# Kernel optimization log

Hardware: AMD Instinct MI355X
Metric: run time of the kernel (lower is better)

The kernel has to match this reference:

```python
import jax, jax.numpy as jnp
import numpy as np

B, T, K, H = 2, 2048, 1024, 16


def setup_inputs() -> dict:
    key = jax.random.key(0)
    ks = jax.random.split(key, 9)
    sc = 0.02
    return {
        "x": jax.random.normal(ks[0], (B, T, K), dtype=jnp.float32),
        "Wq_w": jax.random.normal(ks[1], (K, K), dtype=jnp.float32) * sc,
        "Wq_b": jax.random.normal(ks[2], (K,), dtype=jnp.float32) * sc,
        "Wk_w": jax.random.normal(ks[3], (K, K), dtype=jnp.float32) * sc,
        "Wk_b": jax.random.normal(ks[4], (K,), dtype=jnp.float32) * sc,
        "Wv_w": jax.random.normal(ks[5], (K, K), dtype=jnp.float32) * sc,
        "Wv_b": jax.random.normal(ks[6], (K,), dtype=jnp.float32) * sc,
        "Wo_w": jax.random.normal(ks[7], (K, K), dtype=jnp.float32) * sc,
        "Wo_b": jax.random.normal(ks[8], (K,), dtype=jnp.float32) * sc,
    }


def reference(x, Wq_w, Wq_b, Wk_w, Wk_b, Wv_w, Wv_b, Wo_w, Wo_b):
    b, t, k = x.shape
    h = H
    s = k // h
    # nn.Linear: y = x @ W^T + b
    q = x @ Wq_w.T + Wq_b
    kk = x @ Wk_w.T + Wk_b
    v = x @ Wv_w.T + Wv_b
    # [b, t, h, s] -> [b, h, t, s]
    q = q.reshape(b, t, h, s).transpose(0, 2, 1, 3)
    kk = kk.reshape(b, t, h, s).transpose(0, 2, 1, 3)
    v = v.reshape(b, t, h, s).transpose(0, 2, 1, 3)
    # scores [b, h, t, t]
    dot = jnp.einsum("bhqd,bhkd->bhqk", q, kk)
    # causal mask: upper triangle (offset=1) set to -inf BEFORE scaling
    causal = jnp.tril(jnp.ones((t, t), dtype=bool))
    dot = jnp.where(causal, dot, -jnp.inf)
    # NOTE: original scales by sqrt(k) (full model dim), not sqrt(head_dim)
    dot = dot / jnp.sqrt(jnp.asarray(k, dot.dtype))
    attn = jax.nn.softmax(dot, axis=-1)
    out = jnp.einsum("bhqk,bhkd->bhqd", attn, v)  # [b, h, t, s]
    out = out.transpose(0, 2, 1, 3).reshape(b, t, k)
    return out @ Wo_w.T + Wo_b
```

## Files before the change

kernel.cpp:

```cpp
#include <hip/hip_runtime.h>

typedef unsigned short u16;
typedef unsigned int u32;
typedef __bf16 bf16x8 __attribute__((ext_vector_type(8)));
typedef float f32x4 __attribute__((ext_vector_type(4)));
typedef unsigned short u16x8 __attribute__((ext_vector_type(8)));
typedef unsigned int u32x4 __attribute__((ext_vector_type(4)));

#define B_ 2
#define T_ 2048
#define K_ 1024
#define H_ 16
#define S_ 64
#define MKC 4194304
#define QSCALE 0.04508422f

__device__ __forceinline__ u16 f2bf(float f) {
  unsigned int u = __builtin_bit_cast(unsigned int, f);
  u += 0x7fffu + ((u >> 16) & 1u);
  return (u16)(u >> 16);
}

__device__ __forceinline__ f32x4 MFMA(bf16x8 a, bf16x8 b, f32x4 c) {
  return __builtin_amdgcn_mfma_f32_16x16x32_bf16(a, b, c, 0, 0, 0);
}

__device__ __forceinline__ void gld16(const void* g, void* l) {
  __builtin_amdgcn_global_load_lds((const __attribute__((address_space(1))) void*)g,
                                   (__attribute__((address_space(3))) void*)l, 16, 0, 0);
}

template <int N>
__device__ __forceinline__ void waitv() {
  asm volatile("s_waitcnt vmcnt(%0)" ::"i"(N) : "memory");
}
__device__ __forceinline__ void memfence_barrier() {
  asm volatile("" ::: "memory");
  __builtin_amdgcn_s_barrier();
}

__global__ __launch_bounds__(256) void cvt_all(const float* __restrict__ x,
                                               const float* __restrict__ W0,
                                               const float* __restrict__ W1,
                                               const float* __restrict__ W2,
                                               const float* __restrict__ W3,
                                               u16* __restrict__ xb,
                                               u16* __restrict__ wb) {
  const int i = blockIdx.x * 256 + threadIdx.x;
  const float* src;
  u16* dst;
  if (i < 524288) {
    src = x + (size_t)i * 8;
    dst = xb + (size_t)i * 8;
  } else {
    const int j = i - 524288;
    const int sel = j >> 17;
    const float* W = sel == 0 ? W0 : sel == 1 ? W1 : sel == 2 ? W2 : W3;
    src = W + (size_t)(j & 131071) * 8;
    dst = wb + (size_t)j * 8;
  }
  const float4* s = (const float4*)src;
  float4 f0 = s[0], f1 = s[1];
  u16x8 p;
  p[0] = f2bf(f0.x); p[1] = f2bf(f0.y); p[2] = f2bf(f0.z); p[3] = f2bf(f0.w);
  p[4] = f2bf(f1.x); p[5] = f2bf(f1.y); p[6] = f2bf(f1.z); p[7] = f2bf(f1.w);
  *(u16x8*)dst = p;
}

template <int OMODE, int BN>
__global__ __launch_bounds__(256) void gemm16(const u16* __restrict__ A,
                                              const u16* __restrict__ Bm,
                                              const float* __restrict__ b0,
                                              const float* __restrict__ b1,
                                              const float* __restrict__ b2,
                                              void* __restrict__ C0,
                                              int M, int N, int K) {
  constexpr int NF = BN / 32;
  constexpr int SOPS = 2 + BN / 64;
  __shared__ u16 As[2][128 * 32];
  __shared__ u16 Bs[2][BN * 32];
  const int bm = blockIdx.x * 128;
  const int bn = blockIdx.y * BN;
  const int tid = threadIdx.x;
  const int w = tid >> 6, lane = tid & 63;
  const int wr = (w >> 1) * 64, wc = (w & 1) * (BN / 2);
  const int lr = lane & 15, g = lane >> 4;
  const int lk = (g ^ ((lr >> 1) & 3)) * 8;
  const int srow = lane >> 2;
  const int scol = ((lane & 3) ^ ((lane >> 3) & 3)) * 8;

  f32x4 acc[4][NF] = {};

  auto stg = [&](int buf, int k0) {
#pragma unroll
    for (int i = 0; i < 2; ++i) {
      const int rbase = (i * 4 + w) * 16;
      gld16(A + (size_t)(bm + rbase + srow) * K + k0 + scol, &As[buf][rbase * 32]);
    }
#pragma unroll
    for (int i = 0; i < BN / 64; ++i) {
      const int rbase = (i * 4 + w) * 16;
      gld16(Bm + (size_t)(bn + rbase + srow) * K + k0 + scol, &Bs[buf][rbase * 32]);
    }
  };

  stg(0, 0);
  const int NK = K >> 5;
  for (int kk = 0; kk < NK; ++kk) {
    const int buf = kk & 1;
    const bool pf = (kk + 1 < NK);
    if (pf) {
      stg(buf ^ 1, (kk + 1) * 32);
      waitv<SOPS>();
    } else {
      waitv<0>();
    }
    __builtin_amdgcn_s_barrier();
    bf16x8 af[4], bfr[NF];
#pragma unroll
    for (int m = 0; m < 4; ++m)
      af[m] = *(const bf16x8*)&As[buf][(wr + m * 16 + lr) * 32 + lk];
#pragma unroll
    for (int n = 0; n < NF; ++n)
      bfr[n] = *(const bf16x8*)&Bs[buf][(wc + n * 16 + lr) * 32 + lk];
#pragma unroll
    for (int m = 0; m < 4; ++m)
#pragma unroll
      for (int n = 0; n < NF; ++n)
        acc[m][n] = MFMA(af[m], bfr[n], acc[m][n]);
    memfence_barrier();
  }

  const int sel = (OMODE == 2) ? 0 : (bn >> 10);
  const float* bp = (OMODE == 2) ? b0 : (sel == 0 ? b0 : sel == 1 ? b1 : b2);
#pragma unroll
  for (int n = 0; n < NF; ++n) {
    const int col = bn + wc + n * 16 + lr;
    const float bv = bp[(OMODE == 2) ? col : (col & 1023)];
#pragma unroll
    for (int m = 0; m < 4; ++m) {
#pragma unroll
      for (int r = 0; r < 4; ++r) {
        const int row = bm + wr + m * 16 + g * 4 + r;
        float v = acc[m][n][r] + bv;
        if (OMODE == 2) {
          ((float*)C0)[(size_t)row * N + col] = v;
        } else {
          u16* dst = (u16*)C0;
          const int cc = col & 1023;
          if (sel == 2) {
            const int bb = row >> 11, t = row & 2047, hh = cc >> 6, ss = cc & 63;
            dst[(size_t)2 * MKC + (((size_t)(bb * H_ + hh) * S_ + ss) << 11) + t] = f2bf(v);
          } else {
            if (sel == 0) v *= QSCALE;
            dst[(size_t)sel * MKC + (size_t)row * 1024 + cc] = f2bf(v);
          }
        }
      }
    }
  }
}

__global__ __launch_bounds__(256) void attn_fwd(const u16* __restrict__ Q,
                                                const u16* __restrict__ Kb,
                                                const u16* __restrict__ Vt,
                                                u16* __restrict__ O) {
  __shared__ u16 Ks[2][64 * 64];
  __shared__ u16 Vs[2][64 * 64];
  const int tid = threadIdx.x;
  const int w = tid >> 6, lane = tid & 63;
  const int qh = lane & 15;
  const int g = lane >> 4;
  const int bh = blockIdx.x;
  const int b = bh >> 4, h = bh & 15;
  const int yy = blockIdx.y;

  const int srow = lane >> 3;
  const int sl8 = ((lane & 7) ^ srow) * 8;
  int kvp[2];
#pragma unroll
  for (int i = 0; i < 2; ++i) {
    const int rho = w * 16 + i * 8 + srow;
    const int a = rho >> 4;
    kvp[i] = ((a >> 1) << 5) | (((rho >> 2) & 3) << 3) | ((a & 1) << 2) | (rho & 3);
  }
  const int ksw = qh & 7;
  u16x8 ov;
#pragma unroll
  for (int i = 0; i < 8; ++i) ov[i] = 0x3F80;
  const bf16x8 ones = __builtin_bit_cast(bf16x8, ov);

  for (int seg = 0; seg < 2; ++seg) {
    const int qtile = seg ? (31 - yy) : yy;
    const int qb = qtile * 64;
    const int qw = qb + w * 16;
    const int myq = qw + qh;
    const int nk = qtile + 1;

    const size_t qoff = (size_t)(b * T_ + qw + qh) * K_ + h * S_ + g * 8;
    const bf16x8 bq0 = *(const bf16x8*)(Q + qoff);
    const bf16x8 bq1 = *(const bf16x8*)(Q + qoff + 32);

    const u16* kq0 = Kb + (size_t)(b * T_ + kvp[0]) * K_ + h * S_ + sl8;
    const u16* kq1 = Kb + (size_t)(b * T_ + kvp[1]) * K_ + h * S_ + sl8;
    const u16* vq0 = Vt + (size_t)(bh * S_ + w * 16 + srow) * T_ + sl8;
    const u16* vq1 = Vt + (size_t)(bh * S_ + w * 16 + 8 + srow) * T_ + sl8;

    auto stageK = [&](int buf) {
      gld16(kq0, &Ks[buf][(w * 16) * 64]);
      gld16(kq1, &Ks[buf][(w * 16 + 8) * 64]);
      kq0 += 64 * K_; kq1 += 64 * K_;
    };
    auto stageV = [&](int buf) {
      gld16(vq0, &Vs[buf][(w * 16) * 64]);
      gld16(vq1, &Vs[buf][(w * 16 + 8) * 64]);
      vq0 += 64; vq1 += 64;
    };

    f32x4 o[4] = {};
    f32x4 o_l = {};
    f32x4 sA[4], sB[4];

    auto QKT = [&](int buf, f32x4 (&sO)[4]) {
      __builtin_amdgcn_s_setprio(1);
#pragma unroll
      for (int a = 0; a < 4; ++a) {
        const u16* kr = &Ks[buf][(a * 16 + qh) * 64];
        const bf16x8 kf0 = *(const bf16x8*)(kr + ((g ^ ksw) * 8));
        const bf16x8 kf1 = *(const bf16x8*)(kr + (((4 + g) ^ ksw) * 8));
        f32x4 z = {0.f, 0.f, 0.f, 0.f};
        z = MFMA(kf0, bq0, z);
        sO[a] = MFMA(kf1, bq1, z);
      }
      __builtin_amdgcn_s_setprio(0);
    };

    auto SMPV = [&](f32x4 (&sIn)[4], int buf, int k0) {
      float p[4][4];
      if (k0 + 63 > qw) {
        const int thr = myq - k0 - (g << 3);
#pragma unroll
        for (int a = 0; a < 4; ++a)
#pragma unroll
          for (int r = 0; r < 4; ++r) {
            const int C = ((a >> 1) << 5) + ((a & 1) << 2) + r;
            p[a][r] = (C <= thr) ? __builtin_amdgcn_exp2f(sIn[a][r]) : 0.f;
          }
      } else {
#pragma unroll
        for (int a = 0; a < 4; ++a)
#pragma unroll
          for (int r = 0; r < 4; ++r)
            p[a][r] = __builtin_amdgcn_exp2f(sIn[a][r]);
      }

      __builtin_amdgcn_s_setprio(1);
#pragma unroll
      for (int c = 0; c < 2; ++c) {
        u32 t0, t1, t2, t3;
        asm("v_cvt_pk_bf16_f32 %0, %1, %2" : "=v"(t0) : "v"(p[2 * c][0]), "v"(p[2 * c][1]));
        asm("v_cvt_pk_bf16_f32 %0, %1, %2" : "=v"(t1) : "v"(p[2 * c][2]), "v"(p[2 * c][3]));
        asm("v_cvt_pk_bf16_f32 %0, %1, %2" : "=v"(t2) : "v"(p[2 * c + 1][0]), "v"(p[2 * c + 1][1]));
        asm("v_cvt_pk_bf16_f32 %0, %1, %2" : "=v"(t3) : "v"(p[2 * c + 1][2]), "v"(p[2 * c + 1][3]));
        u32x4 tv; tv[0] = t0; tv[1] = t1; tv[2] = t2; tv[3] = t3;
        const bf16x8 pa = __builtin_bit_cast(bf16x8, tv);
        o_l = MFMA(pa, ones, o_l);
#pragma unroll
        for (int nn = 0; nn < 4; ++nn) {
          const bf16x8 vf =
              *(const bf16x8*)(&Vs[buf][(16 * nn + qh) * 64] + (((c * 4 + g) ^ ksw) * 8));
          o[nn] = MFMA(pa, vf, o[nn]);
        }
      }
      __builtin_amdgcn_s_setprio(0);
    };

    stageK(0); stageV(0);
    waitv<0>();
    __builtin_amdgcn_s_barrier();
    QKT(0, sA);
    if (nk > 1) { stageK(1); stageV(1); }

    int kt = 0;
    for (;;) {
      {
        const bool hn = kt + 1 < nk;
        if (hn) waitv<2>(); else waitv<0>();
        __builtin_amdgcn_s_barrier();
        if (hn) { QKT(1, sB); if (kt + 2 < nk) stageK(0); }
        SMPV(sA, 0, kt * 64);
        memfence_barrier();
        if (kt + 2 < nk) stageV(0);
        if (!hn) break;
        ++kt;
      }
      {
        const bool hn = kt + 1 < nk;
        if (hn) waitv<2>(); else waitv<0>();
        __builtin_amdgcn_s_barrier();
        if (hn) { QKT(0, sA); if (kt + 2 < nk) stageK(1); }
        SMPV(sB, 1, kt * 64);
        memfence_barrier();
        if (kt + 2 < nk) stageV(1);
        if (!hn) break;
        ++kt;
      }
    }

#pragma unroll
    for (int r = 0; r < 4; ++r) {
      const float inv = 1.f / o_l[r];
      const size_t row = (size_t)(b * T_ + qw + 4 * g + r);
#pragma unroll
      for (int nn = 0; nn < 4; ++nn)
        O[row * K_ + h * S_ + nn * 16 + qh] = f2bf(o[nn][r] * inv);
    }
  }
}

extern "C" void kernel_launch(void* const* d_in, const int* in_sizes, int n_in,
                              void* d_out, int out_size, void* d_ws, size_t ws_size,
                              hipStream_t stream) {
  (void)in_sizes; (void)n_in; (void)out_size; (void)ws_size;
  const float* x  = (const float*)d_in[0];
  const float* Wq = (const float*)d_in[1];
  const float* bq = (const float*)d_in[2];
  const float* Wk = (const float*)d_in[3];
  const float* bk = (const float*)d_in[4];
  const float* Wv = (const float*)d_in[5];
  const float* bv = (const float*)d_in[6];
  const float* Wo = (const float*)d_in[7];
  const float* bo = (const float*)d_in[8];
  float* out = (float*)d_out;

  const size_t MK = (size_t)MKC;
  const size_t WK = (size_t)K_ * K_;
  u16* Qb  = (u16*)d_ws;
  u16* Kbf = Qb + MK;
  u16* Vtb = Kbf + MK;
  u16* AO  = Vtb + MK;
  u16* xb  = AO + MK;
  u16* Wqkv = xb + MK;
  u16* Wob  = Wqkv + 3 * WK;

  dim3 blk(256);
  cvt_all<<<dim3(4096), blk, 0, stream>>>(x, Wq, Wk, Wv, Wo, xb, Wqkv);
  gemm16<3, 128><<<dim3(32, 24), blk, 0, stream>>>(xb, Wqkv, bq, bk, bv, Qb,
                                                   B_ * T_, 3 * K_, K_);
  attn_fwd<<<dim3(B_ * H_, 16), blk, 0, stream>>>(Qb, Kbf, Vtb, AO);
  gemm16<2, 64><<<dim3(32, 16), blk, 0, stream>>>(AO, Wob, bo, bo, bo, out,
                                                  B_ * T_, K_, K_);
}
```

Measured before the change: 98.98 us.

## Process two query tiles per block sharing each staged K/V tile

Instead of running two sequential causal segments (tile yy and 31-yy), each block now handles query tiles y and y+16 together and streams K/V once, reusing each staged tile for both query tiles while the lower one is still active. This cuts redundant K/V global loads for the overlapping prefix. The software pipeline is simplified to a single combined K+V stage per iteration with prefetch of the next tile, dropping the earlier QK^T/softmax interleave across tiles. It also doubles the output accumulators held in registers, and the pairing requires gridDim.y of 16.

```diff
diff --git a/kernel.cpp b/kernel.cpp
--- a/kernel.cpp
+++ b/kernel.cpp
@@ -174,6 +174,18 @@
   const int bh = blockIdx.x;
   const int b = bh >> 4, h = bh & 15;
   const int yy = blockIdx.y;
+  const int y = (yy < 8) ? yy : 23 - yy;
+  const int nkA = y + 1, nkB = y + 17;
+  const int qwA = y * 64 + w * 16;
+  const int qwB = (y + 16) * 64 + w * 16;
+  const int myqA = qwA + qh, myqB = qwB + qh;
+
+  const size_t qoffA = (size_t)(b * T_ + qwA + qh) * K_ + h * S_ + g * 8;
+  const bf16x8 bqA0 = *(const bf16x8*)(Q + qoffA);
+  const bf16x8 bqA1 = *(const bf16x8*)(Q + qoffA + 32);
+  const size_t qoffB = (size_t)(b * T_ + qwB + qh) * K_ + h * S_ + g * 8;
+  const bf16x8 bqB0 = *(const bf16x8*)(Q + qoffB);
+  const bf16x8 bqB1 = *(const bf16x8*)(Q + qoffB + 32);
 
   const int srow = lane >> 3;
   const int sl8 = ((lane & 7) ^ srow) * 8;
@@ -190,131 +202,115 @@
   for (int i = 0; i < 8; ++i) ov[i] = 0x3F80;
   const bf16x8 ones = __builtin_bit_cast(bf16x8, ov);
 
-  for (int seg = 0; seg < 2; ++seg) {
-    const int qtile = seg ? (31 - yy) : yy;
-    const int qb = qtile * 64;
-    const int qw = qb + w * 16;
-    const int myq = qw + qh;
-    const int nk = qtile + 1;
-
-    const size_t qoff = (size_t)(b * T_ + qw + qh) * K_ + h * S_ + g * 8;
-    const bf16x8 bq0 = *(const bf16x8*)(Q + qoff);
-    const bf16x8 bq1 = *(const bf16x8*)(Q + qoff + 32);
-
-    const u16* kq0 = Kb + (size_t)(b * T_ + kvp[0]) * K_ + h * S_ + sl8;
-    const u16* kq1 = Kb + (size_t)(b * T_ + kvp[1]) * K_ + h * S_ + sl8;
-    const u16* vq0 = Vt + (size_t)(bh * S_ + w * 16 + srow) * T_ + sl8;
-    const u16* vq1 = Vt + (size_t)(bh * S_ + w * 16 + 8 + srow) * T_ + sl8;
-
-    auto stageK = [&](int buf) {
-      gld16(kq0, &Ks[buf][(w * 16) * 64]);
-      gld16(kq1, &Ks[buf][(w * 16 + 8) * 64]);
-      kq0 += 64 * K_; kq1 += 64 * K_;
-    };
-    auto stageV = [&](int buf) {
-      gld16(vq0, &Vs[buf][(w * 16) * 64]);
-      gld16(vq1, &Vs[buf][(w * 16 + 8) * 64]);
-      vq0 += 64; vq1 += 64;
-    };
-
-    f32x4 o[4] = {};
-    f32x4 o_l = {};
-    f32x4 sA[4], sB[4];
-
-    auto QKT = [&](int buf, f32x4 (&sO)[4]) {
-      __builtin_amdgcn_s_setprio(1);
-#pragma unroll
-      for (int a = 0; a < 4; ++a) {
-        const u16* kr = &Ks[buf][(a * 16 + qh) * 64];
-        const bf16x8 kf0 = *(const bf16x8*)(kr + ((g ^ ksw) * 8));
-        const bf16x8 kf1 = *(const bf16x8*)(kr + (((4 + g) ^ ksw) * 8));
-        f32x4 z = {0.f, 0.f, 0.f, 0.f};
-        z = MFMA(kf0, bq0, z);
-        sO[a] = MFMA(kf1, bq1, z);
+  const u16* kq0 = Kb + (size_t)(b * T_ + kvp[0]) * K_ + h * S_ + sl8;
+  const u16* kq1 = Kb + (size_t)(b * T_ + kvp[1]) * K_ + h * S_ + sl8;
+  const u16* vq0 = Vt + (size_t)(bh * S_ + w * 16 + srow) * T_ + sl8;
+  const u16* vq1 = Vt + (size_t)(bh * S_ + w * 16 + 8 + srow) * T_ + sl8;
+
+  auto stage = [&](int buf) {
+    gld16(kq0, &Ks[buf][(w * 16) * 64]);
+    gld16(kq1, &Ks[buf][(w * 16 + 8) * 64]);
+    gld16(vq0, &Vs[buf][(w * 16) * 64]);
+    gld16(vq1, &Vs[buf][(w * 16 + 8) * 64]);
+    kq0 += 64 * K_; kq1 += 64 * K_; vq0 += 64; vq1 += 64;
+  };
+
+  f32x4 oA[4] = {}, oB[4] = {};
+  f32x4 olA = {}, olB = {};
+
+  auto QKT = [&](int buf, f32x4 (&sO)[4], bf16x8 q0, bf16x8 q1) {
+    __builtin_amdgcn_s_setprio(1);
+#pragma unroll
+    for (int a = 0; a < 4; ++a) {
+      const u16* kr = &Ks[buf][(a * 16 + qh) * 64];
+      const bf16x8 kf0 = *(const bf16x8*)(kr + ((g ^ ksw) * 8));
+      const bf16x8 kf1 = *(const bf16x8*)(kr + (((4 + g) ^ ksw) * 8));
+      f32x4 z = {0.f, 0.f, 0.f, 0.f};
+      z = MFMA(kf0, q0, z);
+      sO[a] = MFMA(kf1, q1, z);
+    }
+    __builtin_amdgcn_s_setprio(0);
+  };
+
+  auto SMPV = [&](f32x4 (&sIn)[4], int buf, int k0, int qw, int myq,
+                  f32x4 (&o)[4], f32x4& ol) {
+    float p[4][4];
+    if (k0 + 63 > qw) {
+      const int thr = myq - k0 - (g << 3);
+#pragma unroll
+      for (int a = 0; a < 4; ++a)
+#pragma unroll
+        for (int r = 0; r < 4; ++r) {
+          const int C = ((a >> 1) << 5) + ((a & 1) << 2) + r;
+          p[a][r] = (C <= thr) ? __builtin_amdgcn_exp2f(sIn[a][r]) : 0.f;
+        }
+    } else {
+#pragma unroll
+      for (int a = 0; a < 4; ++a)
+#pragma unroll
+        for (int r = 0; r < 4; ++r)
+          p[a][r] = __builtin_amdgcn_exp2f(sIn[a][r]);
+    }
+
+    __builtin_amdgcn_s_setprio(1);
+#pragma unroll
+    for (int c = 0; c < 2; ++c) {
+      u32 t0, t1, t2, t3;
+      asm("v_cvt_pk_bf16_f32 %0, %1, %2" : "=v"(t0) : "v"(p[2 * c][0]), "v"(p[2 * c][1]));
+      asm("v_cvt_pk_bf16_f32 %0, %1, %2" : "=v"(t1) : "v"(p[2 * c][2]), "v"(p[2 * c][3]));
+      asm("v_cvt_pk_bf16_f32 %0, %1, %2" : "=v"(t2) : "v"(p[2 * c + 1][0]), "v"(p[2 * c + 1][1]));
+      asm("v_cvt_pk_bf16_f32 %0, %1, %2" : "=v"(t3) : "v"(p[2 * c + 1][2]), "v"(p[2 * c + 1][3]));
+      u32x4 tv; tv[0] = t0; tv[1] = t1; tv[2] = t2; tv[3] = t3;
+      const bf16x8 pa = __builtin_bit_cast(bf16x8, tv);
+      ol = MFMA(pa, ones, ol);
+#pragma unroll
+      for (int nn = 0; nn < 4; ++nn) {
+        const bf16x8 vf =
+            *(const bf16x8*)(&Vs[buf][(16 * nn + qh) * 64] + (((c * 4 + g) ^ ksw) * 8));
+        o[nn] = MFMA(pa, vf, o[nn]);
       }
-      __builtin_amdgcn_s_setprio(0);
-    };
-
-    auto SMPV = [&](f32x4 (&sIn)[4], int buf, int k0) {
-      float p[4][4];
-      if (k0 + 63 > qw) {
-        const int thr = myq - k0 - (g << 3);
-#pragma unroll
-        for (int a = 0; a < 4; ++a)
-#pragma unroll
-          for (int r = 0; r < 4; ++r) {
-            const int C = ((a >> 1) << 5) + ((a & 1) << 2) + r;
-            p[a][r] = (C <= thr) ? __builtin_amdgcn_exp2f(sIn[a][r]) : 0.f;
-          }
-      } else {
-#pragma unroll
-        for (int a = 0; a < 4; ++a)
-#pragma unroll
-          for (int r = 0; r < 4; ++r)
-            p[a][r] = __builtin_amdgcn_exp2f(sIn[a][r]);
-      }
-
-      __builtin_amdgcn_s_setprio(1);
-#pragma unroll
-      for (int c = 0; c < 2; ++c) {
-        u32 t0, t1, t2, t3;
-        asm("v_cvt_pk_bf16_f32 %0, %1, %2" : "=v"(t0) : "v"(p[2 * c][0]), "v"(p[2 * c][1]));
-        asm("v_cvt_pk_bf16_f32 %0, %1, %2" : "=v"(t1) : "v"(p[2 * c][2]), "v"(p[2 * c][3]));
-        asm("v_cvt_pk_bf16_f32 %0, %1, %2" : "=v"(t2) : "v"(p[2 * c + 1][0]), "v"(p[2 * c + 1][1]));
-        asm("v_cvt_pk_bf16_f32 %0, %1, %2" : "=v"(t3) : "v"(p[2 * c + 1][2]), "v"(p[2 * c + 1][3]));
-        u32x4 tv; tv[0] = t0; tv[1] = t1; tv[2] = t2; tv[3] = t3;
-        const bf16x8 pa = __builtin_bit_cast(bf16x8, tv);
-        o_l = MFMA(pa, ones, o_l);
-#pragma unroll
-        for (int nn = 0; nn < 4; ++nn) {
-          const bf16x8 vf =
-              *(const bf16x8*)(&Vs[buf][(16 * nn + qh) * 64] + (((c * 4 + g) ^ ksw) * 8));
-          o[nn] = MFMA(pa, vf, o[nn]);
-        }
-      }
-      __builtin_amdgcn_s_setprio(0);
-    };
-
-    stageK(0); stageV(0);
-    waitv<0>();
+    }
+    __builtin_amdgcn_s_setprio(0);
+  };
+
+  stage(0);
+  for (int kt = 0; kt < nkB; ++kt) {
+    const int cur = kt & 1;
+    const bool hn = kt + 1 < nkB;
+    if (hn) {
+      stage(cur ^ 1);
+      waitv<4>();
+    } else {
+      waitv<0>();
+    }
     __builtin_amdgcn_s_barrier();
-    QKT(0, sA);
-    if (nk > 1) { stageK(1); stageV(1); }
-
-    int kt = 0;
-    for (;;) {
-      {
-        const bool hn = kt + 1 < nk;
-        if (hn) waitv<2>(); else waitv<0>();
-        __builtin_amdgcn_s_barrier();
-        if (hn) { QKT(1, sB); if (kt + 2 < nk) stageK(0); }
-        SMPV(sA, 0, kt * 64);
-        memfence_barrier();
-        if (kt + 2 < nk) stageV(0);
-        if (!hn) break;
-        ++kt;
-      }
-      {
-        const bool hn = kt + 1 < nk;
-        if (hn) waitv<2>(); else waitv<0>();
-        __builtin_amdgcn_s_barrier();
-        if (hn) { QKT(0, sA); if (kt + 2 < nk) stageK(1); }
-        SMPV(sB, 1, kt * 64);
-        memfence_barrier();
-        if (kt + 2 < nk) stageV(1);
-        if (!hn) break;
-        ++kt;
-      }
-    }
-
-#pragma unroll
-    for (int r = 0; r < 4; ++r) {
-      const float inv = 1.f / o_l[r];
-      const size_t row = (size_t)(b * T_ + qw + 4 * g + r);
-#pragma unroll
-      for (int nn = 0; nn < 4; ++nn)
-        O[row * K_ + h * S_ + nn * 16 + qh] = f2bf(o[nn][r] * inv);
-    }
+
+    if (kt < nkA) {
+      f32x4 s4[4];
+      QKT(cur, s4, bqA0, bqA1);
+      SMPV(s4, cur, kt * 64, qwA, myqA, oA, olA);
+    }
+    {
+      f32x4 s4[4];
+      QKT(cur, s4, bqB0, bqB1);
+      SMPV(s4, cur, kt * 64, qwB, myqB, oB, olB);
+    }
+
+    memfence_barrier();
+  }
+
+#pragma unroll
+  for (int r = 0; r < 4; ++r) {
+    const float invA = 1.f / olA[r];
+    const size_t rowA = (size_t)(b * T_ + qwA + 4 * g + r);
+#pragma unroll
+    for (int nn = 0; nn < 4; ++nn)
+      O[rowA * K_ + h * S_ + nn * 16 + qh] = f2bf(oA[nn][r] * invA);
+    const float invB = 1.f / olB[r];
+    const size_t rowB = (size_t)(b * T_ + qwB + 4 * g + r);
+#pragma unroll
+    for (int nn = 0; nn < 4; ++nn)
+      O[rowB * K_ + h * S_ + nn * 16 + qh] = f2bf(oB[nn][r] * invB);
   }
 }
 
```

Result: slower. 105.6 us (+6.7%).
